# Kernel optimization log

Hardware: AMD Instinct MI355X
Metric: run time of the kernel (lower is better)

Reference implementation:

```python
import jax, jax.numpy as jnp
import numpy as np

D, H, KV, HD, F = 2048, 16, 4, 128, 5632
WIN, NG = 512, 64          # sliding window size, num global tokens
EPS = 1e-6
KEEP_ATTN = 1.0 - 0.82     # Ramanujan sparsity on attention projections
KEEP_FFN = 1.0 - 0.88      # Ramanujan sparsity on FFN projections


def _mask_w(key, shape, keep):
    """Fixed structured-sparse weight: dense init * binary keep-mask."""
    k1, k2 = jax.random.split(key)
    w = jax.random.normal(k1, shape, dtype=jnp.float32) * (shape[0] ** -0.5)
    m = (jax.random.uniform(k2, shape) < keep).astype(jnp.float32)
    return w * m


def setup_inputs() -> dict:
    key = jax.random.key(0)
    ks = jax.random.split(key, 8)
    x = jax.random.normal(ks[0], (1, 2048, D), dtype=jnp.float32)
    return {
        "x": x,
        "g_attn": jnp.ones((D,), jnp.float32),   # RMSNorm weight (attn)
        "g_ffn": jnp.ones((D,), jnp.float32),    # RMSNorm weight (ffn)
        "wq": _mask_w(ks[1], (D, H * HD), KEEP_ATTN),
        "wk": _mask_w(ks[2], (D, KV * HD), KEEP_ATTN),
        "wv": _mask_w(ks[3], (D, KV * HD), KEEP_ATTN),
        "wo": _mask_w(ks[4], (H * HD, D), KEEP_ATTN),
        "w1": _mask_w(ks[5], (D, F), KEEP_FFN),   # SwiGLU gate proj
        "w3": _mask_w(ks[6], (D, F), KEEP_FFN),   # SwiGLU up proj
        "w2": _mask_w(ks[7], (F, D), KEEP_FFN),   # SwiGLU down proj
    }


def _rmsnorm(x, g):
    return x * jax.lax.rsqrt(jnp.mean(x * x, axis=-1, keepdims=True) + EPS) * g


def _qknorm(t):  # RMS-normalize over head_dim (QK-Normalization)
    return t * jax.lax.rsqrt(jnp.mean(t * t, axis=-1, keepdims=True) + EPS)


def reference(x, g_attn, g_ffn, wq, wk, wv, wo, w1, w2, w3):
    B, S, _ = x.shape
    # --- attention sub-block: x = x + SlidingWindowGQA(RMSNorm(x)) ---
    h = _rmsnorm(x, g_attn)
    q = h @ wq
    q = q.reshape(B, S, H, HD)
    k = (h @ wk).reshape(B, S, KV, HD)
    v = (h @ wv).reshape(B, S, KV, HD)
    q, k = _qknorm(q), _qknorm(k)
    rep = H // KV
    k = jnp.repeat(k, rep, axis=2)  # [B,S,H,HD]
    v = jnp.repeat(v, rep, axis=2)
    scores = jnp.einsum("bihd,bjhd->bhij", q, k) * (HD ** -0.5)
    # causal + (sliding window OR global row OR global column)
    i = jnp.arange(S)[:, None]
    j = jnp.arange(S)[None, :]
    allowed = (j <= i) & (((i - j) < WIN) | (j < NG) | (i < NG))
    scores = jnp.where(allowed[None, None], scores, jnp.float32(-1e30))
    attn = jax.nn.softmax(scores, axis=-1)
    o = jnp.einsum("bhij,bjhd->bihd", attn, v).reshape(B, S, H * HD)
    x = x + o @ wo
    # --- FFN sub-block: x = x + SparseSwiGLU(RMSNorm(x)) ---
    h2 = _rmsnorm(x, g_ffn)
    ffn = (jax.nn.silu(h2 @ w1) * (h2 @ w3)) @ w2
    return x + ffn
```

## Files before the change

kernel.cpp:

```cpp
#include <hip/hip_runtime.h>
#include <hip/hip_bf16.h>
#include <stdint.h>

typedef _Float16 fp16_t;
typedef __attribute__((ext_vector_type(8))) _Float16 fp16x8;
typedef __attribute__((ext_vector_type(4))) _Float16 fp16x4;
typedef __attribute__((ext_vector_type(2))) _Float16 fp16x2;
typedef __attribute__((ext_vector_type(4))) float f32x4;

#define WIN 512
#define NG 64

__device__ __forceinline__ void gload16(const void* g, void* l) {
    __builtin_amdgcn_global_load_lds((const __attribute__((address_space(1))) void*)g,
                                     (__attribute__((address_space(3))) void*)l, 16, 0, 0);
}

__device__ __forceinline__ void tr_tile(const float* __restrict__ src, int C, int srow, int scol,
                                        fp16_t* __restrict__ out, int R, int orow) {
    __shared__ fp16_t t[64][66];
    int tid = threadIdx.x;
    int tx = tid & 15, ty = tid >> 4;
#pragma unroll
    for (int j = 0; j < 4; ++j) {
        int r = ty + j * 16;
        float4 v = *(const float4*)&src[(size_t)(srow + r) * C + scol + tx * 4];
        fp16x2 a = { (fp16_t)v.x, (fp16_t)v.y };
        fp16x2 b = { (fp16_t)v.z, (fp16_t)v.w };
        *(fp16x2*)&t[r][tx * 4] = a;
        *(fp16x2*)&t[r][tx * 4 + 2] = b;
    }
    __syncthreads();
#pragma unroll
    for (int jj = 0; jj < 4; ++jj) {
        int c = ty + jj * 16;
        fp16x4 o = { t[tx * 4 + 0][c], t[tx * 4 + 1][c], t[tx * 4 + 2][c], t[tx * 4 + 3][c] };
        *(fp16x4*)&out[(size_t)(orow + c) * R + srow + tx * 4] = o;
    }
}

__global__ __launch_bounds__(256) void transpose_qkv3(const float* __restrict__ wq,
                                                      const float* __restrict__ wk,
                                                      const float* __restrict__ wv,
                                                      fp16_t* __restrict__ out) {
    int n0 = blockIdx.x * 64, k0 = blockIdx.y * 64;
    const float* src; int C, c0;
    if (n0 < 2048)      { src = wq; C = 2048; c0 = n0; }
    else if (n0 < 2560) { src = wk; C = 512;  c0 = n0 - 2048; }
    else                { src = wv; C = 512;  c0 = n0 - 2560; }
    tr_tile(src, C, k0, c0, out, 2048, n0);
}

__global__ __launch_bounds__(256) void transpose_w13(const float* __restrict__ w1,
                                                     const float* __restrict__ w3,
                                                     fp16_t* __restrict__ o1,
                                                     fp16_t* __restrict__ o3) {
    const float* src = blockIdx.z ? w3 : w1;
    fp16_t* out = blockIdx.z ? o3 : o1;
    tr_tile(src, 5632, blockIdx.y * 64, blockIdx.x * 64, out, 2048, blockIdx.x * 64);
}

__global__ __launch_bounds__(256) void transpose_one(const float* __restrict__ src,
                                                     fp16_t* __restrict__ out, int R, int C) {
    tr_tile(src, C, blockIdx.y * 64, blockIdx.x * 64, out, R, blockIdx.x * 64);
}

__global__ __launch_bounds__(256) void rmsnorm_kernel(const float* __restrict__ in,
                                                      const float* __restrict__ g,
                                                      fp16_t* __restrict__ out) {
    int row = blockIdx.x;
    int tid = threadIdx.x;
    const float4* rp = (const float4*)(in + (size_t)row * 2048);
    float4 v0 = rp[tid], v1 = rp[tid + 256];
    float ss = v0.x * v0.x + v0.y * v0.y + v0.z * v0.z + v0.w * v0.w +
               v1.x * v1.x + v1.y * v1.y + v1.z * v1.z + v1.w * v1.w;
#pragma unroll
    for (int m = 1; m < 64; m <<= 1) ss += __shfl_xor(ss, m);
    __shared__ float red[4];
    if ((tid & 63) == 0) red[tid >> 6] = ss;
    __syncthreads();
    ss = red[0] + red[1] + red[2] + red[3];
    float sc = rsqrtf(ss * (1.0f / 2048.0f) + 1e-6f);
    const float4* gp = (const float4*)g;
    float4 g0 = gp[tid], g1 = gp[tid + 256];
    fp16x4 o0 = { (fp16_t)(v0.x * sc * g0.x), (fp16_t)(v0.y * sc * g0.y),
                  (fp16_t)(v0.z * sc * g0.z), (fp16_t)(v0.w * sc * g0.w) };
    fp16x4 o1 = { (fp16_t)(v1.x * sc * g1.x), (fp16_t)(v1.y * sc * g1.y),
                  (fp16_t)(v1.z * sc * g1.z), (fp16_t)(v1.w * sc * g1.w) };
    *(fp16x4*)(out + (size_t)row * 2048 + tid * 4) = o0;
    *(fp16x4*)(out + (size_t)row * 2048 + 1024 + tid * 4) = o1;
}

__global__ __launch_bounds__(256) void rmsnorm_add2(const float* __restrict__ xin,
                                                    const float* __restrict__ p0,
                                                    const float* __restrict__ p1,
                                                    const float* __restrict__ g,
                                                    float* __restrict__ x1out,
                                                    fp16_t* __restrict__ hout) {
    int row = blockIdx.x;
    int tid = threadIdx.x;
    size_t base = (size_t)row * 2048;
    const float4* xp = (const float4*)(xin + base);
    const float4* ap = (const float4*)(p0 + base);
    const float4* bp = (const float4*)(p1 + base);
    float4 v0 = xp[tid], v1 = xp[tid + 256];
    float4 a0 = ap[tid], a1 = ap[tid + 256];
    float4 b0 = bp[tid], b1 = bp[tid + 256];
    v0.x += a0.x + b0.x; v0.y += a0.y + b0.y; v0.z += a0.z + b0.z; v0.w += a0.w + b0.w;
    v1.x += a1.x + b1.x; v1.y += a1.y + b1.y; v1.z += a1.z + b1.z; v1.w += a1.w + b1.w;
    float ss = v0.x * v0.x + v0.y * v0.y + v0.z * v0.z + v0.w * v0.w +
               v1.x * v1.x + v1.y * v1.y + v1.z * v1.z + v1.w * v1.w;
#pragma unroll
    for (int m = 1; m < 64; m <<= 1) ss += __shfl_xor(ss, m);
    __shared__ float red[4];
    if ((tid & 63) == 0) red[tid >> 6] = ss;
    __syncthreads();
    ss = red[0] + red[1] + red[2] + red[3];
    float sc = rsqrtf(ss * (1.0f / 2048.0f) + 1e-6f);
    ((float4*)(x1out + base))[tid] = v0;
    ((float4*)(x1out + base))[tid + 256] = v1;
    const float4* gp = (const float4*)g;
    float4 g0 = gp[tid], g1 = gp[tid + 256];
    fp16x4 o0 = { (fp16_t)(v0.x * sc * g0.x), (fp16_t)(v0.y * sc * g0.y),
                  (fp16_t)(v0.z * sc * g0.z), (fp16_t)(v0.w * sc * g0.w) };
    fp16x4 o1 = { (fp16_t)(v1.x * sc * g1.x), (fp16_t)(v1.y * sc * g1.y),
                  (fp16_t)(v1.z * sc * g1.z), (fp16_t)(v1.w * sc * g1.w) };
    *(fp16x4*)(hout + base + tid * 4) = o0;
    *(fp16x4*)(hout + base + 1024 + tid * 4) = o1;
}

__global__ __launch_bounds__(256) void final_add2(float* __restrict__ out,
                                                  const float* __restrict__ p0,
                                                  const float* __restrict__ p1) {
    size_t i = (size_t)blockIdx.x * 256 + threadIdx.x;
    float4 o = ((const float4*)out)[i];
    float4 a = ((const float4*)p0)[i];
    float4 b = ((const float4*)p1)[i];
    o.x += a.x + b.x; o.y += a.y + b.y; o.z += a.z + b.z; o.w += a.w + b.w;
    ((float4*)out)[i] = o;
}

#define BM 128
#define BN 128
#define BKK 64

struct GemmCore {
    int tid, lane, wid, lo, hi, wr, wc;
    int arow[4], ascb[4];
    __device__ __forceinline__ void init(int t) {
        tid = t; lane = t & 63; wid = t >> 6;
        lo = lane & 15; hi = lane >> 4;
        wr = (wid >> 1) * 64; wc = (wid & 1) * 64;
#pragma unroll
        for (int p = 0; p < 4; ++p) {
            int idx = (wid * 4 + p) * 64 + lane;
            int row = idx >> 3;
            int cb = (idx & 7) << 4;
            arow[p] = row;
            ascb[p] = cb ^ ((row & 7) << 4);
        }
    }
    __device__ __forceinline__ void stage(char* buf, const fp16_t* A, const fp16_t* Bt,
                                          int brow, int bcol, int lda, int ldb, int kb) {
        char* As = buf;
        char* Bs = buf + 16384;
#pragma unroll
        for (int p = 0; p < 4; ++p) {
            int ci = wid * 4 + p;
            gload16((const char*)A + ((size_t)(brow + arow[p]) * lda + kb) * 2 + ascb[p],
                    As + ci * 1024);
            gload16((const char*)Bt + ((size_t)(bcol + arow[p]) * ldb + kb) * 2 + ascb[p],
                    Bs + ci * 1024);
        }
    }
    __device__ __forceinline__ void compute(const char* buf, f32x4 (&acc)[4][4]) {
        const char* As = buf;
        const char* Bs = buf + 16384;
#pragma unroll
        for (int kc = 0; kc < 2; ++kc) {
            fp16x8 af[4], bfr[4];
            int boff = kc * 64 + hi * 16;
#pragma unroll
            for (int m = 0; m < 4; ++m) {
                int row = wr + m * 16 + lo;
                af[m] = *(const fp16x8*)(As + row * 128 + (boff ^ ((row & 7) << 4)));
            }
#pragma unroll
            for (int n = 0; n < 4; ++n) {
                int row = wc + n * 16 + lo;
                bfr[n] = *(const fp16x8*)(Bs + row * 128 + (boff ^ ((row & 7) << 4)));
            }
#pragma unroll
            for (int m = 0; m < 4; ++m)
#pragma unroll
                for (int n = 0; n < 4; ++n)
                    acc[m][n] = __builtin_amdgcn_mfma_f32_16x16x32_f16(af[m], bfr[n], acc[m][n], 0, 0, 0);
        }
    }
};

template <int EPI>
__global__ __launch_bounds__(256, 2) void gemm_bt(const fp16_t* __restrict__ A,
                                                  const fp16_t* __restrict__ Bt,
                                                  void* __restrict__ Cout,
                                                  const float* __restrict__ resid,
                                                  fp16_t* __restrict__ vT,
                                                  int M, int N, int K,
                                                  int lda, int ldb, int ksplit) {
    __shared__ __align__(16) char smem[2][32768];
    GemmCore g;
    g.init(threadIdx.x);
    int brow = blockIdx.y * BM, bcol = blockIdx.x * BN;

    int Kloc = K / ksplit;
    int kbase0 = blockIdx.z * Kloc;
    int nK = Kloc / BKK;

    f32x4 acc[4][4] = {};
    g.stage(smem[0], A, Bt, brow, bcol, lda, ldb, kbase0);
    __syncthreads();
    for (int kt = 0; kt < nK; ++kt) {
        if (kt + 1 < nK) g.stage(smem[(kt + 1) & 1], A, Bt, brow, bcol, lda, ldb,
                                 kbase0 + (kt + 1) * BKK);
        g.compute(smem[kt & 1], acc);
        __syncthreads();
    }

    if (EPI == 3) {
        if (blockIdx.x < 20) {
            float* sq = (float*)smem;
            bool isq = blockIdx.x < 16;
#pragma unroll
            for (int m = 0; m < 4; ++m)
#pragma unroll
                for (int r = 0; r < 4; ++r) {
                    float s = 0.f;
#pragma unroll
                    for (int n = 0; n < 4; ++n) s += acc[m][n][r] * acc[m][n][r];
                    s += __shfl_xor(s, 1); s += __shfl_xor(s, 2);
                    s += __shfl_xor(s, 4); s += __shfl_xor(s, 8);
                    if (g.lo == 0) sq[g.wid * 64 + m * 16 + g.hi * 4 + r] = s;
                }
            __syncthreads();
#pragma unroll
            for (int m = 0; m < 4; ++m)
#pragma unroll
                for (int r = 0; r < 4; ++r) {
                    int rl = m * 16 + g.hi * 4 + r;
                    float tot = sq[g.wid * 64 + rl] + sq[(g.wid ^ 1) * 64 + rl];
                    float sc = rsqrtf(tot * (1.0f / 128.0f) + 1e-6f);
                    if (isq) sc *= 0.08838834764831843f;
#pragma unroll
                    for (int n = 0; n < 4; ++n) acc[m][n][r] *= sc;
                }
        } else {
#pragma unroll
            for (int m = 0; m < 4; ++m) {
                int gcol0 = brow + g.wr + m * 16 + g.hi * 4;
#pragma unroll
                for (int n = 0; n < 4; ++n) {
                    int vrow = bcol + g.wc + n * 16 + g.lo - 2560;
                    fp16x4 o = { (fp16_t)acc[m][n][0], (fp16_t)acc[m][n][1],
                                 (fp16_t)acc[m][n][2], (fp16_t)acc[m][n][3] };
                    *(fp16x4*)&vT[(size_t)vrow * 2048 + gcol0] = o;
                }
            }
            return;
        }
    }

#pragma unroll
    for (int m = 0; m < 4; ++m) {
        int grow0 = brow + g.wr + m * 16 + g.hi * 4;
#pragma unroll
        for (int n = 0; n < 4; ++n) {
            int gcol = bcol + g.wc + n * 16 + g.lo;
#pragma unroll
            for (int r = 0; r < 4; ++r) {
                size_t gidx = (size_t)(grow0 + r) * N + gcol;
                float v = acc[m][n][r];
                if (EPI == 0 || EPI == 3) {
                    ((fp16_t*)Cout)[gidx] = (fp16_t)v;
                } else if (EPI == 1) {
                    ((float*)Cout)[gidx] = v + resid[gidx];
                } else {
                    ((float*)Cout)[(size_t)blockIdx.z * M * N + gidx] = v;
                }
            }
        }
    }
}

__global__ __launch_bounds__(256, 2) void gemm_u1u3_half(const fp16_t* __restrict__ A,
                                                         const fp16_t* __restrict__ Bt1,
                                                         const fp16_t* __restrict__ Bt3,
                                                         fp16_t* __restrict__ G,
                                                         int M, int N, int K) {
    __shared__ __align__(16) char smem[2][32768];
    int tid = threadIdx.x, lane = tid & 63, wid = tid >> 6;
    int lo = lane & 15, hi = lane >> 4;
    int wr = (wid >> 1) * 64, wc = (wid & 1) * 32;
    int brow = blockIdx.y * 128, bcol = blockIdx.x * 64;
    int nK = K / BKK;

    int arow[4], ascb[4];
#pragma unroll
    for (int p = 0; p < 4; ++p) {
        int idx = (wid * 4 + p) * 64 + lane;
        int row = idx >> 3;
        int cb = (idx & 7) << 4;
        arow[p] = row;
        ascb[p] = cb ^ ((row & 7) << 4);
    }
    int brow_[2], bscb[2];
#pragma unroll
    for (int p = 0; p < 2; ++p) {
        int idx = (wid * 2 + p) * 64 + lane;
        int row = idx >> 3;
        int cb = (idx & 7) << 4;
        brow_[p] = row;
        bscb[p] = cb ^ ((row & 7) << 4);
    }

    auto stage = [&](char* buf, int kb) {
        char* As = buf;
        char* B1s = buf + 16384;
        char* B3s = buf + 24576;
#pragma unroll
        for (int p = 0; p < 4; ++p)
            gload16((const char*)A + ((size_t)(brow + arow[p]) * K + kb) * 2 + ascb[p],
                    As + (wid * 4 + p) * 1024);
#pragma unroll
        for (int p = 0; p < 2; ++p) {
            gload16((const char*)Bt1 + ((size_t)(bcol + brow_[p]) * K + kb) * 2 + bscb[p],
                    B1s + (wid * 2 + p) * 1024);
            gload16((const char*)Bt3 + ((size_t)(bcol + brow_[p]) * K + kb) * 2 + bscb[p],
                    B3s + (wid * 2 + p) * 1024);
        }
    };

    f32x4 acc1[4][2] = {}, acc3[4][2] = {};
    stage(smem[0], 0);
    __syncthreads();
    for (int kt = 0; kt < nK; ++kt) {
        if (kt + 1 < nK) stage(smem[(kt + 1) & 1], (kt + 1) * BKK);
        const char* As = smem[kt & 1];
        const char* B1s = As + 16384;
        const char* B3s = As + 24576;
#pragma unroll
        for (int kc = 0; kc < 2; ++kc) {
            fp16x8 af[4], b1f[2], b3f[2];
            int boff = kc * 64 + hi * 16;
#pragma unroll
            for (int m = 0; m < 4; ++m) {
                int row = wr + m * 16 + lo;
                af[m] = *(const fp16x8*)(As + row * 128 + (boff ^ ((row & 7) << 4)));
            }
#pragma unroll
            for (int n = 0; n < 2; ++n) {
                int row = wc + n * 16 + lo;
                int o = row * 128 + (boff ^ ((row & 7) << 4));
                b1f[n] = *(const fp16x8*)(B1s + o);
                b3f[n] = *(const fp16x8*)(B3s + o);
            }
#pragma unroll
            for (int m = 0; m < 4; ++m)
#pragma unroll
                for (int n = 0; n < 2; ++n) {
                    acc1[m][n] = __builtin_amdgcn_mfma_f32_16x16x32_f16(af[m], b1f[n], acc1[m][n], 0, 0, 0);
                    acc3[m][n] = __builtin_amdgcn_mfma_f32_16x16x32_f16(af[m], b3f[n], acc3[m][n], 0, 0, 0);
                }
        }
        __syncthreads();
    }

#pragma unroll
    for (int m = 0; m < 4; ++m) {
        int grow0 = brow + wr + m * 16 + hi * 4;
#pragma unroll
        for (int n = 0; n < 2; ++n) {
            int gcol = bcol + wc + n * 16 + lo;
#pragma unroll
            for (int r = 0; r < 4; ++r) {
                float u = acc1[m][n][r];
                float val = (u / (1.0f + __expf(-u))) * acc3[m][n][r];
                G[(size_t)(grow0 + r) * N + gcol] = (fp16_t)val;
            }
        }
    }
}

__global__ __launch_bounds__(256, 2) void attn_kernel(const fp16_t* __restrict__ qkv,
                                                      const fp16_t* __restrict__ vT,
                                                      fp16_t* __restrict__ o) {
    __shared__ __align__(16) char smem[16384 + 16384 + 4 * 2304];
    char* Ks = smem;
    char* VTs = smem + 16384;
    char* Ps = smem + 32768;

    int t = blockIdx.x, qh = blockIdx.y;
    int kvh = qh >> 2;
    int qs = t * 64;
    int tid = threadIdx.x, lane = tid & 63, wid = tid >> 6;
    int lo = lane & 15, hi = lane >> 4;

    fp16x8 qf[4];
    {
        const fp16_t* qptr = qkv + (size_t)(qs + wid * 16 + lo) * 3072 + qh * 128 + hi * 8;
#pragma unroll
        for (int kc = 0; kc < 4; ++kc) qf[kc] = *(const fp16x8*)(qptr + kc * 32);
    }

    f32x4 oacc[8] = {};
    float m_r[4], l_r[4];
#pragma unroll
    for (int r = 0; r < 4; ++r) { m_r[r] = -1e30f; l_r[r] = 0.0f; }

    int lot = qs - (WIN - 1);
    int jt_lo = lot <= 0 ? 0 : (lot >> 6);
    int nt = (jt_lo > 0) ? (t - jt_lo + 2) : (t + 1);

    for (int ti = 0; ti < nt; ++ti) {
        int jt = (jt_lo > 0) ? (ti == 0 ? 0 : jt_lo + ti - 1) : ti;
        int js = jt * 64;
        __syncthreads();
#pragma unroll
        for (int p = 0; p < 4; ++p) {
            int ci = wid * 4 + p;
            int idx = ci * 64 + lane;
            int krow = idx >> 4;
            int kcb = (idx & 15) << 4;
            int kscb = kcb ^ ((krow & 7) << 4);
            gload16((const char*)qkv + ((size_t)(js + krow) * 3072 + 2048 + kvh * 128) * 2 + kscb,
                    Ks + ci * 1024);
            int vrow = idx >> 3;
            int vcb = (idx & 7) << 4;
            int vscb = vcb ^ ((vrow & 7) << 4);
            gload16((const char*)vT + ((size_t)(kvh * 128 + vrow) * 2048 + js) * 2 + vscb,
                    VTs + ci * 1024);
        }
        __syncthreads();

        f32x4 s[4] = {};
#pragma unroll
        for (int kc = 0; kc < 4; ++kc) {
#pragma unroll
            for (int jc = 0; jc < 4; ++jc) {
                int row = jc * 16 + lo;
                fp16x8 kf = *(const fp16x8*)(Ks + row * 256 + ((kc * 64 + hi * 16) ^ ((row & 7) << 4)));
                s[jc] = __builtin_amdgcn_mfma_f32_16x16x32_f16(qf[kc], kf, s[jc], 0, 0, 0);
            }
        }

        float mt[4] = { -1e30f, -1e30f, -1e30f, -1e30f };
#pragma unroll
        for (int jc = 0; jc < 4; ++jc) {
            int j = js + jc * 16 + lo;
#pragma unroll
            for (int r = 0; r < 4; ++r) {
                int i = qs + wid * 16 + hi * 4 + r;
                bool ok = (j <= i) && (((i - j) < WIN) || (j < NG) || (i < NG));
                float sv = ok ? s[jc][r] : -1e30f;
                s[jc][r] = sv;
                mt[r] = fmaxf(mt[r], sv);
            }
        }
#pragma unroll
        for (int m2 = 1; m2 <= 8; m2 <<= 1)
#pragma unroll
            for (int r = 0; r < 4; ++r) mt[r] = fmaxf(mt[r], __shfl_xor(mt[r], m2));
        float sf[4], psum[4];
#pragma unroll
        for (int r = 0; r < 4; ++r) {
            float mn = fmaxf(m_r[r], mt[r]);
            sf[r] = __expf(m_r[r] - mn);
            m_r[r] = mn;
            psum[r] = 0.0f;
        }
#pragma unroll
        for (int jc = 0; jc < 4; ++jc)
#pragma unroll
            for (int r = 0; r < 4; ++r) {
                float p = __expf(s[jc][r] - m_r[r]);
                s[jc][r] = p;
                psum[r] += p;
            }
#pragma unroll
        for (int m2 = 1; m2 <= 8; m2 <<= 1)
#pragma unroll
            for (int r = 0; r < 4; ++r) psum[r] += __shfl_xor(psum[r], m2);
#pragma unroll
        for (int r = 0; r < 4; ++r) l_r[r] = l_r[r] * sf[r] + psum[r];
#pragma unroll
        for (int nc = 0; nc < 8; ++nc)
#pragma unroll
            for (int r = 0; r < 4; ++r) oacc[nc][r] *= sf[r];

        char* Pb = Ps + wid * 2304;
#pragma unroll
        for (int jc = 0; jc < 4; ++jc)
#pragma unroll
            for (int r = 0; r < 4; ++r)
                *(fp16_t*)(Pb + (hi * 4 + r) * 144 + (jc * 16 + lo) * 2) = (fp16_t)s[jc][r];
        fp16x8 pa[2];
#pragma unroll
        for (int jc2 = 0; jc2 < 2; ++jc2)
            pa[jc2] = *(const fp16x8*)(Pb + lo * 144 + jc2 * 64 + hi * 16);

#pragma unroll
        for (int jc2 = 0; jc2 < 2; ++jc2)
#pragma unroll
            for (int nc = 0; nc < 8; ++nc) {
                int row = nc * 16 + lo;
                fp16x8 vf = *(const fp16x8*)(VTs + row * 128 + ((jc2 * 64 + hi * 16) ^ ((row & 7) << 4)));
                oacc[nc] = __builtin_amdgcn_mfma_f32_16x16x32_f16(pa[jc2], vf, oacc[nc], 0, 0, 0);
            }
    }

#pragma unroll
    for (int r = 0; r < 4; ++r) {
        float inv = 1.0f / l_r[r];
        int orow = qs + wid * 16 + hi * 4 + r;
#pragma unroll
        for (int nc = 0; nc < 8; ++nc)
            o[(size_t)orow * 2048 + qh * 128 + nc * 16 + lo] = (fp16_t)(oacc[nc][r] * inv);
    }
}

extern "C" void kernel_launch(void* const* d_in, const int* in_sizes, int n_in,
                              void* d_out, int out_size, void* d_ws, size_t ws_size,
                              hipStream_t stream) {
    const float* x = (const float*)d_in[0];
    const float* g_attn = (const float*)d_in[1];
    const float* g_ffn = (const float*)d_in[2];
    const float* wq = (const float*)d_in[3];
    const float* wk = (const float*)d_in[4];
    const float* wv = (const float*)d_in[5];
    const float* wo = (const float*)d_in[6];
    const float* w1 = (const float*)d_in[7];
    const float* w3 = (const float*)d_in[8];
    const float* w2 = (const float*)d_in[9];
    float* out = (float*)d_out;

    char* ws = (char*)d_ws;
    size_t off = 0;
    auto alloc = [&](size_t bytes) {
        char* p = ws + off;
        off += (bytes + 255) & ~(size_t)255;
        return p;
    };
    fp16_t* hbuf  = (fp16_t*)alloc(2048ull * 2048 * 2);
    fp16_t* wqkvT = (fp16_t*)alloc(3072ull * 2048 * 2);
    fp16_t* vTb   = (fp16_t*)alloc(512ull * 2048 * 2);
    fp16_t* qkv   = (fp16_t*)alloc(2048ull * 3072 * 2);
    fp16_t* gbuf  = (fp16_t*)alloc(2048ull * 5632 * 2);
    float*  part  = (float*)alloc(2ull * 2048 * 2048 * 4);
    fp16_t* wbigT = (fp16_t*)alloc(5632ull * 2048 * 2);
    if (off > ws_size) {
        hipMemsetAsync(d_out, 0, (size_t)out_size * 4, stream);
        return;
    }
    float* part1 = part + 2048ull * 2048;
    fp16_t* w3T = hbuf;

    transpose_qkv3<<<dim3(48, 32), 256, 0, stream>>>(wq, wk, wv, wqkvT);
    rmsnorm_kernel<<<2048, 256, 0, stream>>>(x, g_attn, hbuf);
    gemm_bt<3><<<dim3(24, 16, 1), 256, 0, stream>>>(hbuf, wqkvT, qkv, nullptr, vTb,
                                                    2048, 3072, 2048, 2048, 2048, 1);
    attn_kernel<<<dim3(32, 16), 256, 0, stream>>>(qkv, vTb, hbuf);
    transpose_one<<<dim3(32, 32), 256, 0, stream>>>(wo, wqkvT, 2048, 2048);
    gemm_bt<2><<<dim3(16, 16, 2), 256, 0, stream>>>(hbuf, wqkvT, part, nullptr, nullptr,
                                                    2048, 2048, 2048, 2048, 2048, 2);
    rmsnorm_add2<<<2048, 256, 0, stream>>>(x, part, part1, g_ffn, out, qkv);
    transpose_w13<<<dim3(88, 32, 2), 256, 0, stream>>>(w1, w3, wbigT, w3T);
    gemm_u1u3_half<<<dim3(88, 16), 256, 0, stream>>>(qkv, wbigT, w3T, gbuf, 2048, 5632, 2048);
    transpose_one<<<dim3(32, 88), 256, 0, stream>>>(w2, wbigT, 5632, 2048);
    gemm_bt<2><<<dim3(16, 16, 2), 256, 0, stream>>>(gbuf, wbigT, part, nullptr, nullptr,
                                                    2048, 2048, 5632, 5632, 5632, 2);
    final_add2<<<4096, 256, 0, stream>>>(out, part, part1);
}
```

Measured before the change: 306.6 us.

## Replace split-K GEMMs with 128x64-tile GEMM fusing residual add epilogue

Both output GEMMs (wo and w2) previously used split-K=2 with 128x128 tiles, writing two fp32 partial buffers that separate kernels (rmsnorm_add2, final_add2) then summed. They now use a new 128x64-tile kernel without split-K that adds the residual directly in the epilogue. The plain rmsnorm kernel is then reused on the result. This removes the partial-buffer traffic and two elementwise kernels, and keeps 512 blocks through smaller tiles. The cost is more B-operand reloads per FLOP and a long K loop for the w2 GEMM.

```diff
diff --git a/kernel.cpp b/kernel.cpp
--- a/kernel.cpp
+++ b/kernel.cpp
@@ -91,55 +91,6 @@
     *(fp16x4*)(out + (size_t)row * 2048 + 1024 + tid * 4) = o1;
 }
 
-__global__ __launch_bounds__(256) void rmsnorm_add2(const float* __restrict__ xin,
-                                                    const float* __restrict__ p0,
-                                                    const float* __restrict__ p1,
-                                                    const float* __restrict__ g,
-                                                    float* __restrict__ x1out,
-                                                    fp16_t* __restrict__ hout) {
-    int row = blockIdx.x;
-    int tid = threadIdx.x;
-    size_t base = (size_t)row * 2048;
-    const float4* xp = (const float4*)(xin + base);
-    const float4* ap = (const float4*)(p0 + base);
-    const float4* bp = (const float4*)(p1 + base);
-    float4 v0 = xp[tid], v1 = xp[tid + 256];
-    float4 a0 = ap[tid], a1 = ap[tid + 256];
-    float4 b0 = bp[tid], b1 = bp[tid + 256];
-    v0.x += a0.x + b0.x; v0.y += a0.y + b0.y; v0.z += a0.z + b0.z; v0.w += a0.w + b0.w;
-    v1.x += a1.x + b1.x; v1.y += a1.y + b1.y; v1.z += a1.z + b1.z; v1.w += a1.w + b1.w;
-    float ss = v0.x * v0.x + v0.y * v0.y + v0.z * v0.z + v0.w * v0.w +
-               v1.x * v1.x + v1.y * v1.y + v1.z * v1.z + v1.w * v1.w;
-#pragma unroll
-    for (int m = 1; m < 64; m <<= 1) ss += __shfl_xor(ss, m);
-    __shared__ float red[4];
-    if ((tid & 63) == 0) red[tid >> 6] = ss;
-    __syncthreads();
-    ss = red[0] + red[1] + red[2] + red[3];
-    float sc = rsqrtf(ss * (1.0f / 2048.0f) + 1e-6f);
-    ((float4*)(x1out + base))[tid] = v0;
-    ((float4*)(x1out + base))[tid + 256] = v1;
-    const float4* gp = (const float4*)g;
-    float4 g0 = gp[tid], g1 = gp[tid + 256];
-    fp16x4 o0 = { (fp16_t)(v0.x * sc * g0.x), (fp16_t)(v0.y * sc * g0.y),
-                  (fp16_t)(v0.z * sc * g0.z), (fp16_t)(v0.w * sc * g0.w) };
-    fp16x4 o1 = { (fp16_t)(v1.x * sc * g1.x), (fp16_t)(v1.y * sc * g1.y),
-                  (fp16_t)(v1.z * sc * g1.z), (fp16_t)(v1.w * sc * g1.w) };
-    *(fp16x4*)(hout + base + tid * 4) = o0;
-    *(fp16x4*)(hout + base + 1024 + tid * 4) = o1;
-}
-
-__global__ __launch_bounds__(256) void final_add2(float* __restrict__ out,
-                                                  const float* __restrict__ p0,
-                                                  const float* __restrict__ p1) {
-    size_t i = (size_t)blockIdx.x * 256 + threadIdx.x;
-    float4 o = ((const float4*)out)[i];
-    float4 a = ((const float4*)p0)[i];
-    float4 b = ((const float4*)p1)[i];
-    o.x += a.x + b.x; o.y += a.y + b.y; o.z += a.z + b.z; o.w += a.w + b.w;
-    ((float4*)out)[i] = o;
-}
-
 #define BM 128
 #define BN 128
 #define BKK 64
@@ -199,93 +150,162 @@
     }
 };
 
-template <int EPI>
-__global__ __launch_bounds__(256, 2) void gemm_bt(const fp16_t* __restrict__ A,
-                                                  const fp16_t* __restrict__ Bt,
-                                                  void* __restrict__ Cout,
-                                                  const float* __restrict__ resid,
-                                                  fp16_t* __restrict__ vT,
-                                                  int M, int N, int K,
-                                                  int lda, int ldb, int ksplit) {
+__global__ __launch_bounds__(256, 2) void gemm_qkv(const fp16_t* __restrict__ A,
+                                                   const fp16_t* __restrict__ Bt,
+                                                   fp16_t* __restrict__ Cout,
+                                                   fp16_t* __restrict__ vT,
+                                                   int M, int N, int K) {
     __shared__ __align__(16) char smem[2][32768];
     GemmCore g;
     g.init(threadIdx.x);
     int brow = blockIdx.y * BM, bcol = blockIdx.x * BN;
-
-    int Kloc = K / ksplit;
-    int kbase0 = blockIdx.z * Kloc;
-    int nK = Kloc / BKK;
+    int nK = K / BKK;
 
     f32x4 acc[4][4] = {};
-    g.stage(smem[0], A, Bt, brow, bcol, lda, ldb, kbase0);
+    g.stage(smem[0], A, Bt, brow, bcol, K, K, 0);
     __syncthreads();
     for (int kt = 0; kt < nK; ++kt) {
-        if (kt + 1 < nK) g.stage(smem[(kt + 1) & 1], A, Bt, brow, bcol, lda, ldb,
-                                 kbase0 + (kt + 1) * BKK);
+        if (kt + 1 < nK) g.stage(smem[(kt + 1) & 1], A, Bt, brow, bcol, K, K, (kt + 1) * BKK);
         g.compute(smem[kt & 1], acc);
         __syncthreads();
     }
 
-    if (EPI == 3) {
-        if (blockIdx.x < 20) {
-            float* sq = (float*)smem;
-            bool isq = blockIdx.x < 16;
+    if (blockIdx.x < 20) {
+        float* sq = (float*)smem;
+        bool isq = blockIdx.x < 16;
+#pragma unroll
+        for (int m = 0; m < 4; ++m)
+#pragma unroll
+            for (int r = 0; r < 4; ++r) {
+                float s = 0.f;
+#pragma unroll
+                for (int n = 0; n < 4; ++n) s += acc[m][n][r] * acc[m][n][r];
+                s += __shfl_xor(s, 1); s += __shfl_xor(s, 2);
+                s += __shfl_xor(s, 4); s += __shfl_xor(s, 8);
+                if (g.lo == 0) sq[g.wid * 64 + m * 16 + g.hi * 4 + r] = s;
+            }
+        __syncthreads();
+#pragma unroll
+        for (int m = 0; m < 4; ++m)
+#pragma unroll
+            for (int r = 0; r < 4; ++r) {
+                int rl = m * 16 + g.hi * 4 + r;
+                float tot = sq[g.wid * 64 + rl] + sq[(g.wid ^ 1) * 64 + rl];
+                float sc = rsqrtf(tot * (1.0f / 128.0f) + 1e-6f);
+                if (isq) sc *= 0.08838834764831843f;
+#pragma unroll
+                for (int n = 0; n < 4; ++n) acc[m][n][r] *= sc;
+            }
+#pragma unroll
+        for (int m = 0; m < 4; ++m) {
+            int grow0 = brow + g.wr + m * 16 + g.hi * 4;
+#pragma unroll
+            for (int n = 0; n < 4; ++n) {
+                int gcol = bcol + g.wc + n * 16 + g.lo;
+#pragma unroll
+                for (int r = 0; r < 4; ++r)
+                    Cout[(size_t)(grow0 + r) * N + gcol] = (fp16_t)acc[m][n][r];
+            }
+        }
+    } else {
+#pragma unroll
+        for (int m = 0; m < 4; ++m) {
+            int gcol0 = brow + g.wr + m * 16 + g.hi * 4;
+#pragma unroll
+            for (int n = 0; n < 4; ++n) {
+                int vrow = bcol + g.wc + n * 16 + g.lo - 2560;
+                fp16x4 o = { (fp16_t)acc[m][n][0], (fp16_t)acc[m][n][1],
+                             (fp16_t)acc[m][n][2], (fp16_t)acc[m][n][3] };
+                *(fp16x4*)&vT[(size_t)vrow * 2048 + gcol0] = o;
+            }
+        }
+    }
+}
+
+__global__ __launch_bounds__(256, 2) void gemm_bt64_resid(const fp16_t* __restrict__ A,
+                                                          const fp16_t* __restrict__ Bt,
+                                                          float* __restrict__ Cout,
+                                                          const float* __restrict__ resid,
+                                                          int M, int N, int K) {
+    __shared__ __align__(16) char smem[2][24576];
+    int tid = threadIdx.x, lane = tid & 63, wid = tid >> 6;
+    int lo = lane & 15, hi = lane >> 4;
+    int wr = (wid >> 1) * 64, wc = (wid & 1) * 32;
+    int brow = blockIdx.y * 128, bcol = blockIdx.x * 64;
+    int nK = K / BKK;
+
+    int arow[4], ascb[4];
+#pragma unroll
+    for (int p = 0; p < 4; ++p) {
+        int idx = (wid * 4 + p) * 64 + lane;
+        int row = idx >> 3;
+        int cb = (idx & 7) << 4;
+        arow[p] = row;
+        ascb[p] = cb ^ ((row & 7) << 4);
+    }
+    int brow_[2], bscb[2];
+#pragma unroll
+    for (int p = 0; p < 2; ++p) {
+        int idx = (wid * 2 + p) * 64 + lane;
+        int row = idx >> 3;
+        int cb = (idx & 7) << 4;
+        brow_[p] = row;
+        bscb[p] = cb ^ ((row & 7) << 4);
+    }
+
+    auto stage = [&](char* buf, int kb) {
+        char* As = buf;
+        char* Bs = buf + 16384;
+#pragma unroll
+        for (int p = 0; p < 4; ++p)
+            gload16((const char*)A + ((size_t)(brow + arow[p]) * K + kb) * 2 + ascb[p],
+                    As + (wid * 4 + p) * 1024);
+#pragma unroll
+        for (int p = 0; p < 2; ++p)
+            gload16((const char*)Bt + ((size_t)(bcol + brow_[p]) * K + kb) * 2 + bscb[p],
+                    Bs + (wid * 2 + p) * 1024);
+    };
+
+    f32x4 acc[4][2] = {};
+    stage(smem[0], 0);
+    __syncthreads();
+    for (int kt = 0; kt < nK; ++kt) {
+        if (kt + 1 < nK) stage(smem[(kt + 1) & 1], (kt + 1) * BKK);
+        const char* As = smem[kt & 1];
+        const char* Bs = As + 16384;
+#pragma unroll
+        for (int kc = 0; kc < 2; ++kc) {
+            fp16x8 af[4], bfr[2];
+            int boff = kc * 64 + hi * 16;
+#pragma unroll
+            for (int m = 0; m < 4; ++m) {
+                int row = wr + m * 16 + lo;
+                af[m] = *(const fp16x8*)(As + row * 128 + (boff ^ ((row & 7) << 4)));
+            }
+#pragma unroll
+            for (int n = 0; n < 2; ++n) {
+                int row = wc + n * 16 + lo;
+                bfr[n] = *(const fp16x8*)(Bs + row * 128 + (boff ^ ((row & 7) << 4)));
+            }
 #pragma unroll
             for (int m = 0; m < 4; ++m)
 #pragma unroll
-                for (int r = 0; r < 4; ++r) {
-                    float s = 0.f;
-#pragma unroll
-                    for (int n = 0; n < 4; ++n) s += acc[m][n][r] * acc[m][n][r];
-                    s += __shfl_xor(s, 1); s += __shfl_xor(s, 2);
-                    s += __shfl_xor(s, 4); s += __shfl_xor(s, 8);
-                    if (g.lo == 0) sq[g.wid * 64 + m * 16 + g.hi * 4 + r] = s;
-                }
-            __syncthreads();
-#pragma unroll
-            for (int m = 0; m < 4; ++m)
-#pragma unroll
-                for (int r = 0; r < 4; ++r) {
-                    int rl = m * 16 + g.hi * 4 + r;
-                    float tot = sq[g.wid * 64 + rl] + sq[(g.wid ^ 1) * 64 + rl];
-                    float sc = rsqrtf(tot * (1.0f / 128.0f) + 1e-6f);
-                    if (isq) sc *= 0.08838834764831843f;
-#pragma unroll
-                    for (int n = 0; n < 4; ++n) acc[m][n][r] *= sc;
-                }
-        } else {
-#pragma unroll
-            for (int m = 0; m < 4; ++m) {
-                int gcol0 = brow + g.wr + m * 16 + g.hi * 4;
-#pragma unroll
-                for (int n = 0; n < 4; ++n) {
-                    int vrow = bcol + g.wc + n * 16 + g.lo - 2560;
-                    fp16x4 o = { (fp16_t)acc[m][n][0], (fp16_t)acc[m][n][1],
-                                 (fp16_t)acc[m][n][2], (fp16_t)acc[m][n][3] };
-                    *(fp16x4*)&vT[(size_t)vrow * 2048 + gcol0] = o;
-                }
-            }
-            return;
-        }
+                for (int n = 0; n < 2; ++n)
+                    acc[m][n] = __builtin_amdgcn_mfma_f32_16x16x32_f16(af[m], bfr[n], acc[m][n], 0, 0, 0);
+        }
+        __syncthreads();
     }
 
 #pragma unroll
     for (int m = 0; m < 4; ++m) {
-        int grow0 = brow + g.wr + m * 16 + g.hi * 4;
-#pragma unroll
-        for (int n = 0; n < 4; ++n) {
-            int gcol = bcol + g.wc + n * 16 + g.lo;
+        int grow0 = brow + wr + m * 16 + hi * 4;
+#pragma unroll
+        for (int n = 0; n < 2; ++n) {
+            int gcol = bcol + wc + n * 16 + lo;
 #pragma unroll
             for (int r = 0; r < 4; ++r) {
                 size_t gidx = (size_t)(grow0 + r) * N + gcol;
-                float v = acc[m][n][r];
-                if (EPI == 0 || EPI == 3) {
-                    ((fp16_t*)Cout)[gidx] = (fp16_t)v;
-                } else if (EPI == 1) {
-                    ((float*)Cout)[gidx] = v + resid[gidx];
-                } else {
-                    ((float*)Cout)[(size_t)blockIdx.z * M * N + gidx] = v;
-                }
+                Cout[gidx] = acc[m][n][r] + resid[gidx];
             }
         }
     }
@@ -554,28 +574,22 @@
     fp16_t* vTb   = (fp16_t*)alloc(512ull * 2048 * 2);
     fp16_t* qkv   = (fp16_t*)alloc(2048ull * 3072 * 2);
     fp16_t* gbuf  = (fp16_t*)alloc(2048ull * 5632 * 2);
-    float*  part  = (float*)alloc(2ull * 2048 * 2048 * 4);
     fp16_t* wbigT = (fp16_t*)alloc(5632ull * 2048 * 2);
     if (off > ws_size) {
         hipMemsetAsync(d_out, 0, (size_t)out_size * 4, stream);
         return;
     }
-    float* part1 = part + 2048ull * 2048;
     fp16_t* w3T = hbuf;
 
     transpose_qkv3<<<dim3(48, 32), 256, 0, stream>>>(wq, wk, wv, wqkvT);
     rmsnorm_kernel<<<2048, 256, 0, stream>>>(x, g_attn, hbuf);
-    gemm_bt<3><<<dim3(24, 16, 1), 256, 0, stream>>>(hbuf, wqkvT, qkv, nullptr, vTb,
-                                                    2048, 3072, 2048, 2048, 2048, 1);
+    gemm_qkv<<<dim3(24, 16), 256, 0, stream>>>(hbuf, wqkvT, qkv, vTb, 2048, 3072, 2048);
     attn_kernel<<<dim3(32, 16), 256, 0, stream>>>(qkv, vTb, hbuf);
     transpose_one<<<dim3(32, 32), 256, 0, stream>>>(wo, wqkvT, 2048, 2048);
-    gemm_bt<2><<<dim3(16, 16, 2), 256, 0, stream>>>(hbuf, wqkvT, part, nullptr, nullptr,
-                                                    2048, 2048, 2048, 2048, 2048, 2);
-    rmsnorm_add2<<<2048, 256, 0, stream>>>(x, part, part1, g_ffn, out, qkv);
+    gemm_bt64_resid<<<dim3(32, 16), 256, 0, stream>>>(hbuf, wqkvT, out, x, 2048, 2048, 2048);
+    rmsnorm_kernel<<<2048, 256, 0, stream>>>(out, g_ffn, qkv);
     transpose_w13<<<dim3(88, 32, 2), 256, 0, stream>>>(w1, w3, wbigT, w3T);
     gemm_u1u3_half<<<dim3(88, 16), 256, 0, stream>>>(qkv, wbigT, w3T, gbuf, 2048, 5632, 2048);
     transpose_one<<<dim3(32, 88), 256, 0, stream>>>(w2, wbigT, 5632, 2048);
-    gemm_bt<2><<<dim3(16, 16, 2), 256, 0, stream>>>(gbuf, wbigT, part, nullptr, nullptr,
-                                                    2048, 2048, 5632, 5632, 5632, 2);
-    final_add2<<<4096, 256, 0, stream>>>(out, part, part1);
-}
+    gemm_bt64_resid<<<dim3(32, 16), 256, 0, stream>>>(gbuf, wbigT, out, out, 2048, 2048, 5632);
+}
```

After: 302.9 us. No clear change (-1.2%).
